# Kernel tuning notes

Measured on AMD Instinct MI355X. Metric: run time of the kernel, lower is better.

Reference implementation:

```python
import jax, jax.numpy as jnp
import numpy as np

D_MODEL = 1024
N_HEADS = 16
HEAD_DIM = D_MODEL // N_HEADS
BATCH = 4
SEQ = 2048


def setup_inputs() -> dict:
    key = jax.random.key(0)
    k_x, k_wqkv, k_bqkv, k_wo, k_bo = jax.random.split(key, 5)
    x = jax.random.normal(k_x, (BATCH, SEQ, D_MODEL), dtype=jnp.float32)
    # causal mask: True = masked (upper triangle, excluding diagonal)
    mask = jnp.triu(jnp.ones((SEQ, SEQ), dtype=bool), k=1)
    lim = 1.0 / np.sqrt(D_MODEL)
    w_qkv = jax.random.uniform(k_wqkv, (D_MODEL, 3 * D_MODEL), jnp.float32, -lim, lim)
    b_qkv = jax.random.uniform(k_bqkv, (3 * D_MODEL,), jnp.float32, -lim, lim)
    w_out = jax.random.uniform(k_wo, (D_MODEL, D_MODEL), jnp.float32, -lim, lim)
    b_out = jax.random.uniform(k_bo, (D_MODEL,), jnp.float32, -lim, lim)
    return {"x": x, "mask": mask, "w_qkv": w_qkv, "b_qkv": b_qkv,
            "w_out": w_out, "b_out": b_out}


def reference(x, mask, w_qkv, b_qkv, w_out, b_out):
    b, s, _ = x.shape
    scale = HEAD_DIM ** -0.5
    qkv = x @ w_qkv + b_qkv                          # [b, s, 3*d]
    qkv = qkv.reshape(b, s, 3, N_HEADS, HEAD_DIM)
    qkv = jnp.transpose(qkv, (2, 0, 3, 1, 4))        # [3, b, h, s, hd]
    q, k, v = qkv[0], qkv[1], qkv[2]
    attn = jnp.einsum('bhqd,bhkd->bhqk', q, k) * scale
    attn = jnp.where(mask, -jnp.inf, attn)
    attn = jax.nn.softmax(attn, axis=-1)
    out = jnp.einsum('bhqk,bhkd->bhqd', attn, v)     # [b, h, s, hd]
    out = jnp.transpose(out, (0, 2, 1, 3)).reshape(b, s, D_MODEL)
    return out @ w_out + b_out
```

## Files before the change

kernel.cpp:

```cpp
#include <hip/hip_runtime.h>
#include <stdint.h>

typedef unsigned short u16;
typedef __attribute__((ext_vector_type(8))) short short8;
typedef __attribute__((ext_vector_type(4))) float f32x4;
typedef __attribute__((ext_vector_type(16))) float f32x16;

#define DEV static __device__ __forceinline__

#define QSCALE 0.18033688011112042f

DEV float fast_exp2(float x) { return __builtin_amdgcn_exp2f(x); }

DEV float bf2f(u16 u) { union { uint32_t i; float f; } x; x.i = ((uint32_t)u) << 16; return x.f; }
DEV u16 f2bf(float f) {
  union { float f; uint32_t i; } x; x.f = f;
  uint32_t r = x.i + 0x7FFFu + ((x.i >> 16) & 1u);
  return (u16)(r >> 16);
}
DEV uint32_t pk_bf16(float lo, float hi) {
  uint32_t r;
  asm("v_cvt_pk_bf16_f32 %0, %1, %2" : "=v"(r) : "v"(lo), "v"(hi));
  return r;
}

DEV void async_copy16(void* lds_dst, const void* gsrc) {
  typedef __attribute__((address_space(1))) void* gp_t;
  typedef __attribute__((address_space(3))) void* lp_t;
  __builtin_amdgcn_global_load_lds((gp_t)(uintptr_t)gsrc,
                                   (lp_t)(uint32_t)(uintptr_t)lds_dst, 16, 0, 0);
}

DEV void gemm_bt_core(const u16* __restrict__ A, const u16* __restrict__ Bt, int K,
                      int m0, int n0, uint8_t* As, uint8_t* Bs,
                      f32x4 (&acc)[4][4], int wave, int lane, int wm, int wn) {
#pragma unroll
  for (int mt = 0; mt < 4; ++mt)
#pragma unroll
    for (int nt = 0; nt < 4; ++nt)
      acc[mt][nt] = (f32x4){0.f, 0.f, 0.f, 0.f};

  for (int k0 = 0; k0 < K; k0 += 64) {
    __syncthreads();
#pragma unroll
    for (int i = 0; i < 4; ++i) {
      int cb = wave * 256 + i * 64;
      int c  = cb + lane;
      int r  = c >> 3;
      int ks = (c & 7) ^ (r & 7);
      async_copy16(As + cb * 16 + lane * 16, A  + (size_t)(m0 + r) * K + k0 + ks * 8);
      async_copy16(Bs + cb * 16 + lane * 16, Bt + (size_t)(n0 + r) * K + k0 + ks * 8);
    }
    __syncthreads();

    short8 af[2][4], bf_[2][4];
#pragma unroll
    for (int kk = 0; kk < 2; ++kk)
#pragma unroll
      for (int t = 0; t < 4; ++t) {
        int ra = wm + t * 16 + (lane & 15);
        af[kk][t]  = *(const short8*)(As + ra * 128 + (((kk * 4 + (lane >> 4)) ^ (ra & 7)) << 4));
        int rb = wn + t * 16 + (lane & 15);
        bf_[kk][t] = *(const short8*)(Bs + rb * 128 + (((kk * 4 + (lane >> 4)) ^ (rb & 7)) << 4));
      }
#pragma unroll
    for (int kk = 0; kk < 2; ++kk)
#pragma unroll
      for (int mt = 0; mt < 4; ++mt)
#pragma unroll
        for (int nt = 0; nt < 4; ++nt)
          acc[mt][nt] = __builtin_amdgcn_mfma_f32_16x16x32_bf16(af[kk][mt], bf_[kk][nt],
                                                                acc[mt][nt], 0, 0, 0);
  }
}

__global__ __launch_bounds__(256, 2) void k_gemm_qkv(
    const u16* __restrict__ X, const u16* __restrict__ WT, const float* __restrict__ bias,
    u16* __restrict__ Q, u16* __restrict__ Kv, u16* __restrict__ Vt) {
  __shared__ __attribute__((aligned(16))) uint8_t As[16384];
  __shared__ __attribute__((aligned(16))) uint8_t Bs[16384];
  const int lane = threadIdx.x & 63, wave = threadIdx.x >> 6;
  const int wm = (wave >> 1) * 64, wn = (wave & 1) * 64;
  const int m0 = blockIdx.x * 128, n0 = blockIdx.y * 128;
  f32x4 acc[4][4];
  gemm_bt_core(X, WT, 1024, m0, n0, As, Bs, acc, wave, lane, wm, wn);
#pragma unroll
  for (int nt = 0; nt < 4; ++nt) {
    int n = n0 + wn + nt * 16 + (lane & 15);
    float bv = bias[n];
    int which = n >> 10, h = (n >> 6) & 15, hd = n & 63;
    if (which == 2) {
#pragma unroll
      for (int mt = 0; mt < 4; ++mt) {
        int m = m0 + wm + mt * 16 + (lane >> 4) * 4;
        int b = m >> 11, s = m & 2047;
        u16 tmp[4];
#pragma unroll
        for (int rg = 0; rg < 4; ++rg) tmp[rg] = f2bf(acc[mt][nt][rg] + bv);
        *(uint64_t*)(Vt + ((size_t)(b * 16 + h) * 64 + hd) * 2048 + s) = *(const uint64_t*)tmp;
      }
    } else {
      u16* base = (which == 0) ? Q : Kv;
      const float mul = (which == 0) ? QSCALE : 1.0f;
#pragma unroll
      for (int mt = 0; mt < 4; ++mt)
#pragma unroll
        for (int rg = 0; rg < 4; ++rg) {
          int m = m0 + wm + mt * 16 + (lane >> 4) * 4 + rg;
          int b = m >> 11, s = m & 2047;
          base[((size_t)(b * 16 + h) * 2048 + s) * 64 + hd] = f2bf((acc[mt][nt][rg] + bv) * mul);
        }
    }
  }
}

__global__ __launch_bounds__(256, 2) void k_gemm_out(
    const u16* __restrict__ A, const u16* __restrict__ WT, const float* __restrict__ bias,
    float* __restrict__ Out) {
  __shared__ __attribute__((aligned(16))) uint8_t As[16384];
  __shared__ __attribute__((aligned(16))) uint8_t Bs[16384];
  const int lane = threadIdx.x & 63, wave = threadIdx.x >> 6;
  const int wm = (wave >> 1) * 64, wn = (wave & 1) * 64;
  const int m0 = blockIdx.x * 128, n0 = blockIdx.y * 128;
  f32x4 acc[4][4];
  gemm_bt_core(A, WT, 1024, m0, n0, As, Bs, acc, wave, lane, wm, wn);
#pragma unroll
  for (int nt = 0; nt < 4; ++nt) {
    int n = n0 + wn + nt * 16 + (lane & 15);
    float bv = bias[n];
#pragma unroll
    for (int mt = 0; mt < 4; ++mt)
#pragma unroll
      for (int rg = 0; rg < 4; ++rg) {
        int m = m0 + wm + mt * 16 + (lane >> 4) * 4 + rg;
        Out[(size_t)m * 1024 + n] = acc[mt][nt][rg] + bv;
      }
  }
}

__global__ __launch_bounds__(256) void k_cvt_x(const float* __restrict__ src,
                                               u16* __restrict__ dst, int n8) {
  int i = blockIdx.x * 256 + threadIdx.x;
  if (i >= n8) return;
  float4 a = *(const float4*)(src + (size_t)i * 8);
  float4 b = *(const float4*)(src + (size_t)i * 8 + 4);
  u16 tmp[8] = {f2bf(a.x), f2bf(a.y), f2bf(a.z), f2bf(a.w),
                f2bf(b.x), f2bf(b.y), f2bf(b.z), f2bf(b.w)};
  *(short8*)(dst + (size_t)i * 8) = *(const short8*)tmp;
}

__global__ __launch_bounds__(256) void k_transpose_f32(
    const float* __restrict__ src, u16* __restrict__ dst, int R, int C) {
  __shared__ u16 tile[64][72];
  const int tr = blockIdx.x * 64, tc = blockIdx.y * 64;
  for (int c = threadIdx.x; c < 1024; c += 256) {
    int r = c >> 4, c4 = (c & 15) * 4;
    float4 v = *(const float4*)(src + (size_t)(tr + r) * C + tc + c4);
    tile[r][c4 + 0] = f2bf(v.x); tile[r][c4 + 1] = f2bf(v.y);
    tile[r][c4 + 2] = f2bf(v.z); tile[r][c4 + 3] = f2bf(v.w);
  }
  __syncthreads();
  for (int c = threadIdx.x; c < 512; c += 256) {
    int oc = c >> 3, r8 = (c & 7) * 8;
    u16 tmp[8];
#pragma unroll
    for (int i = 0; i < 8; ++i) tmp[i] = tile[r8 + i][oc];
    *(short8*)(dst + (size_t)(tc + oc) * R + tr + r8) = *(const short8*)tmp;
  }
}

DEV void stage_tile(const u16* __restrict__ Kg, const u16* __restrict__ Vg,
                    uint8_t* kb, uint8_t* vb, int t, int tid) {
#pragma unroll
  for (int i = 0; i < 2; ++i) {
    int c = i * 256 + tid;
    int r = c >> 3;
    int ks = (c & 7) ^ (r & 7);
    async_copy16(kb + c * 16, Kg + (size_t)(t * 64 + r) * 64 + ks * 8);
    async_copy16(vb + c * 16, Vg + (size_t)r * 2048 + t * 64 + ks * 8);
  }
}

__global__ __launch_bounds__(256, 2) void k_attn(
    const u16* __restrict__ Q, const u16* __restrict__ K,
    const u16* __restrict__ Vt, u16* __restrict__ O) {
  __shared__ __attribute__((aligned(16))) uint8_t kbuf[2][8192];
  __shared__ __attribute__((aligned(16))) uint8_t vbuf[2][8192];
  const int tid = threadIdx.x;
  const int lane = tid & 63;
  const int wave = tid >> 6;
  const int q32 = lane & 31, hv = lane >> 5;
  const float NEG_INF = -__builtin_inff();

  int L = blockIdx.x;
  int bh = (L & 7) * 8 + ((L >> 3) >> 3);
  int pair = (L >> 3) & 7;
  const int b = bh >> 4, h = bh & 15;
  const size_t hb = (size_t)bh * (2048 * 64);
  const u16* Qg = Q + hb;
  const u16* Kg = K + hb;
  const u16* Vg = Vt + hb;

#pragma unroll 1
  for (int which = 0; which < 2; ++which) {
    const int s = which ? (15 - pair) : pair;
    const int nt = 2 * (s + 1);
    const int qbase = s * 128 + wave * 32;
    const int qg = qbase + q32;
    const int my_nt = ((qbase + 31) >> 6) + 1;

    short8 qf[4];
#pragma unroll
    for (int dblk = 0; dblk < 4; ++dblk)
      qf[dblk] = *(const short8*)(Qg + (size_t)qg * 64 + dblk * 16 + hv * 8);

    f32x16 oacc[2] = {};
    float mrun = NEG_INF, lrun = 0.f;

    stage_tile(Kg, Vg, kbuf[0], vbuf[0], 0, tid);
    __syncthreads();

#pragma unroll 1
    for (int t = 0; t < nt; ++t) {
      const int cur = t & 1;
      if (t + 1 < nt) stage_tile(Kg, Vg, kbuf[cur ^ 1], vbuf[cur ^ 1], t + 1, tid);

      if (t < my_nt) {
        const uint8_t* kb = kbuf[cur];
        const uint8_t* vb = vbuf[cur];

        f32x16 sa0 = {}, sa1 = {};
        __builtin_amdgcn_s_setprio(1);
#pragma unroll
        for (int dblk = 0; dblk < 4; ++dblk) {
          short8 kf0 = *(const short8*)(kb + q32 * 128 + (((dblk * 2 + hv) ^ (q32 & 7)) << 4));
          short8 kf1 = *(const short8*)(kb + (32 + q32) * 128 + (((dblk * 2 + hv) ^ (q32 & 7)) << 4));
          sa0 = __builtin_amdgcn_mfma_f32_32x32x16_bf16(kf0, qf[dblk], sa0, 0, 0, 0);
          sa1 = __builtin_amdgcn_mfma_f32_32x32x16_bf16(kf1, qf[dblk], sa1, 0, 0, 0);
        }
        __builtin_amdgcn_s_setprio(0);

        float sv[32];
#pragma unroll
        for (int r = 0; r < 16; ++r) { sv[r] = sa0[r]; sv[16 + r] = sa1[r]; }
        if (t * 64 + 63 > qbase) {
#pragma unroll
          for (int r = 0; r < 16; ++r) {
            int kl = (r & 3) + 8 * (r >> 2) + 4 * hv;
            if (t * 64 + kl > qg)      sv[r]      = NEG_INF;
            if (t * 64 + 32 + kl > qg) sv[16 + r] = NEG_INF;
          }
        }

        float mloc = fmaxf(sv[0], sv[1]);
#pragma unroll
        for (int r = 2; r < 32; ++r) mloc = fmaxf(mloc, sv[r]);
        float mtile = fmaxf(mloc, __shfl_xor(mloc, 32, 64));
        if (!__all(mtile <= mrun + 8.f)) {
          float mnew = fmaxf(mrun, mtile);
          float corr = fast_exp2(mrun - mnew);
          mrun = mnew;
          lrun *= corr;
#pragma unroll
          for (int r = 0; r < 16; ++r) { oacc[0][r] *= corr; oacc[1][r] *= corr; }
        }
        float ls = 0.f;
#pragma unroll
        for (int r = 0; r < 32; ++r) { sv[r] = fast_exp2(sv[r] - mrun); ls += sv[r]; }
        ls += __shfl_xor(ls, 32, 64);
        lrun += ls;

        __builtin_amdgcn_s_setprio(1);
#pragma unroll
        for (int ksub = 0; ksub < 2; ++ksub) {
#pragma unroll
          for (int kb2 = 0; kb2 < 2; ++kb2) {
            const int rb = ksub * 16 + kb2 * 8;
            uint32_t pA = pk_bf16(sv[rb + 0], sv[rb + 1]);
            uint32_t pB = pk_bf16(sv[rb + 2], sv[rb + 3]);
            uint32_t pC = pk_bf16(sv[rb + 4], sv[rb + 5]);
            uint32_t pD = pk_bf16(sv[rb + 6], sv[rb + 7]);
            uint32_t X = hv ? pA : pC;
            uint32_t Y = hv ? pB : pD;
            uint32_t sX = (uint32_t)__shfl_xor((int)X, 32, 64);
            uint32_t sY = (uint32_t)__shfl_xor((int)Y, 32, 64);
            union { uint32_t u[4]; short8 s8; } pu;
            pu.u[0] = hv ? sX : pA;
            pu.u[1] = hv ? sY : pB;
            pu.u[2] = hv ? pC : sX;
            pu.u[3] = hv ? pD : sY;
            const int kblk = ksub * 2 + kb2;
            short8 vf0 = *(const short8*)(vb + q32 * 128 + (((kblk * 2 + hv) ^ (q32 & 7)) << 4));
            short8 vf1 = *(const short8*)(vb + (32 + q32) * 128 + (((kblk * 2 + hv) ^ (q32 & 7)) << 4));
            oacc[0] = __builtin_amdgcn_mfma_f32_32x32x16_bf16(vf0, pu.s8, oacc[0], 0, 0, 0);
            oacc[1] = __builtin_amdgcn_mfma_f32_32x32x16_bf16(vf1, pu.s8, oacc[1], 0, 0, 0);
          }
        }
        __builtin_amdgcn_s_setprio(0);
      }

      __syncthreads();
    }

    float rl = 1.0f / lrun;
    u16* orow = O + ((size_t)(b * 2048 + qg)) * 1024 + h * 64;
#pragma unroll
    for (int dt = 0; dt < 2; ++dt)
#pragma unroll
      for (int g = 0; g < 4; ++g) {
        int dbase = dt * 32 + 8 * g + 4 * hv;
        u16 tmp[4];
#pragma unroll
        for (int j = 0; j < 4; ++j) tmp[j] = f2bf(oacc[dt][4 * g + j] * rl);
        *(uint64_t*)(orow + dbase) = *(const uint64_t*)tmp;
      }
  }
}

extern "C" void kernel_launch(void* const* d_in, const int* in_sizes, int n_in,
                              void* d_out, int out_size, void* d_ws, size_t ws_size,
                              hipStream_t stream) {
  const float* x     = (const float*)d_in[0];
  const float* w_qkv = (const float*)d_in[2];
  const float* b_qkv = (const float*)d_in[3];
  const float* w_out = (const float*)d_in[4];
  const float* b_out = (const float*)d_in[5];
  float* out = (float*)d_out;
  uint8_t* ws = (uint8_t*)d_ws;

  u16* wqkvT = (u16*)(ws);
  u16* woutT = (u16*)(ws +  6291456);
  u16* Xb    = (u16*)(ws +  8388608);
  u16* Qb    = (u16*)(ws + 25165824);
  u16* Kb    = (u16*)(ws + 41943040);
  u16* Vtb   = (u16*)(ws + 58720256);
  u16* AO    = Xb;

  k_cvt_x<<<dim3(4096), 256, 0, stream>>>(x, Xb, 1048576);
  k_transpose_f32<<<dim3(16, 48), 256, 0, stream>>>(w_qkv, wqkvT, 1024, 3072);
  k_transpose_f32<<<dim3(16, 16), 256, 0, stream>>>(w_out, woutT, 1024, 1024);
  k_gemm_qkv<<<dim3(64, 24), 256, 0, stream>>>(Xb, wqkvT, b_qkv, Qb, Kb, Vtb);
  k_attn<<<dim3(512), 256, 0, stream>>>(Qb, Kb, Vtb, AO);
  k_gemm_out<<<dim3(64, 8), 256, 0, stream>>>(AO, woutT, b_out, out);
}
```

Baseline: 154.3 us.

## Use 256x128 GEMM tiles with triple-buffered async LDS pipeline

```diff
diff --git a/kernel.cpp b/kernel.cpp
--- a/kernel.cpp
+++ b/kernel.cpp
@@ -31,109 +31,142 @@
                                    (lp_t)(uint32_t)(uintptr_t)lds_dst, 16, 0, 0);
 }
 
-DEV void gemm_bt_core(const u16* __restrict__ A, const u16* __restrict__ Bt, int K,
-                      int m0, int n0, uint8_t* As, uint8_t* Bs,
-                      f32x4 (&acc)[4][4], int wave, int lane, int wm, int wn) {
-#pragma unroll
-  for (int mt = 0; mt < 4; ++mt)
-#pragma unroll
-    for (int nt = 0; nt < 4; ++nt)
-      acc[mt][nt] = (f32x4){0.f, 0.f, 0.f, 0.f};
-
-  for (int k0 = 0; k0 < K; k0 += 64) {
-    __syncthreads();
-#pragma unroll
-    for (int i = 0; i < 4; ++i) {
-      int cb = wave * 256 + i * 64;
-      int c  = cb + lane;
-      int r  = c >> 3;
-      int ks = (c & 7) ^ (r & 7);
-      async_copy16(As + cb * 16 + lane * 16, A  + (size_t)(m0 + r) * K + k0 + ks * 8);
-      async_copy16(Bs + cb * 16 + lane * 16, Bt + (size_t)(n0 + r) * K + k0 + ks * 8);
+#define SLOT_BYTES 49152
+
+DEV void stage_slot(const u16* __restrict__ A, const u16* __restrict__ Bt,
+                    int m0, int n0, int k0, uint8_t* As, uint8_t* Bs, int tid) {
+#pragma unroll
+  for (int i = 0; i < 4; ++i) {
+    int c = i * 512 + tid;
+    int r = c >> 3;
+    int ks = (c & 7) ^ (r & 7);
+    async_copy16(As + c * 16, A + (size_t)(m0 + r) * 1024 + k0 + ks * 8);
+  }
+#pragma unroll
+  for (int i = 0; i < 2; ++i) {
+    int c = i * 512 + tid;
+    int r = c >> 3;
+    int ks = (c & 7) ^ (r & 7);
+    async_copy16(Bs + c * 16, Bt + (size_t)(n0 + r) * 1024 + k0 + ks * 8);
+  }
+}
+
+DEV void gemm256_core(const u16* __restrict__ A, const u16* __restrict__ Bt,
+                      int m0, int n0, uint8_t* lds,
+                      f32x4 (&acc)[4][4], int wave, int lane, int tid) {
+  const int wm = (wave >> 1) * 64, wn = (wave & 1) * 64;
+#pragma unroll
+  for (int mf = 0; mf < 4; ++mf)
+#pragma unroll
+    for (int nf = 0; nf < 4; ++nf)
+      acc[mf][nf] = (f32x4){0.f, 0.f, 0.f, 0.f};
+
+  stage_slot(A, Bt, m0, n0, 0,  lds,              lds + 32768,              tid);
+  stage_slot(A, Bt, m0, n0, 64, lds + SLOT_BYTES, lds + SLOT_BYTES + 32768, tid);
+
+  int cur = 0;
+#pragma unroll 1
+  for (int kt = 0; kt < 16; ++kt) {
+    if (kt + 2 < 16) {
+      int nxt = (cur >= 1) ? cur - 1 : 2;
+      stage_slot(A, Bt, m0, n0, (kt + 2) * 64,
+                 lds + nxt * SLOT_BYTES, lds + nxt * SLOT_BYTES + 32768, tid);
     }
-    __syncthreads();
-
-    short8 af[2][4], bf_[2][4];
-#pragma unroll
-    for (int kk = 0; kk < 2; ++kk)
-#pragma unroll
-      for (int t = 0; t < 4; ++t) {
-        int ra = wm + t * 16 + (lane & 15);
-        af[kk][t]  = *(const short8*)(As + ra * 128 + (((kk * 4 + (lane >> 4)) ^ (ra & 7)) << 4));
-        int rb = wn + t * 16 + (lane & 15);
-        bf_[kk][t] = *(const short8*)(Bs + rb * 128 + (((kk * 4 + (lane >> 4)) ^ (rb & 7)) << 4));
-      }
-#pragma unroll
-    for (int kk = 0; kk < 2; ++kk)
-#pragma unroll
-      for (int mt = 0; mt < 4; ++mt)
-#pragma unroll
-        for (int nt = 0; nt < 4; ++nt)
-          acc[mt][nt] = __builtin_amdgcn_mfma_f32_16x16x32_bf16(af[kk][mt], bf_[kk][nt],
-                                                                acc[mt][nt], 0, 0, 0);
-  }
-}
-
-__global__ __launch_bounds__(256, 2) void k_gemm_qkv(
+    if (kt < 14)       asm volatile("s_waitcnt vmcnt(12)" ::: "memory");
+    else if (kt == 14) asm volatile("s_waitcnt vmcnt(6)"  ::: "memory");
+    else               asm volatile("s_waitcnt vmcnt(0)"  ::: "memory");
+    asm volatile("s_barrier" ::: "memory");
+
+    const uint8_t* Ab = lds + cur * SLOT_BYTES;
+    const uint8_t* Bb = Ab + 32768;
+#pragma unroll
+    for (int kk = 0; kk < 2; ++kk) {
+      short8 af[4], bfr[4];
+#pragma unroll
+      for (int f = 0; f < 4; ++f) {
+        int ra = wm + f * 16 + (lane & 15);
+        af[f]  = *(const short8*)(Ab + ra * 128 + (((kk * 4 + (lane >> 4)) ^ (ra & 7)) << 4));
+      }
+#pragma unroll
+      for (int f = 0; f < 4; ++f) {
+        int rb = wn + f * 16 + (lane & 15);
+        bfr[f] = *(const short8*)(Bb + rb * 128 + (((kk * 4 + (lane >> 4)) ^ (rb & 7)) << 4));
+      }
+      asm volatile("s_barrier" ::: "memory");
+      asm volatile("s_waitcnt lgkmcnt(0)" ::: "memory");
+      __builtin_amdgcn_sched_barrier(0);
+      __builtin_amdgcn_s_setprio(1);
+#pragma unroll
+      for (int mf = 0; mf < 4; ++mf)
+#pragma unroll
+        for (int nf = 0; nf < 4; ++nf)
+          acc[mf][nf] = __builtin_amdgcn_mfma_f32_16x16x32_bf16(af[mf], bfr[nf],
+                                                                acc[mf][nf], 0, 0, 0);
+      __builtin_amdgcn_s_setprio(0);
+      asm volatile("s_barrier" ::: "memory");
+    }
+    cur = (cur == 2) ? 0 : cur + 1;
+  }
+}
+
+__global__ __launch_bounds__(512, 2) void k_gemm_qkv(
     const u16* __restrict__ X, const u16* __restrict__ WT, const float* __restrict__ bias,
     u16* __restrict__ Q, u16* __restrict__ Kv, u16* __restrict__ Vt) {
-  __shared__ __attribute__((aligned(16))) uint8_t As[16384];
-  __shared__ __attribute__((aligned(16))) uint8_t Bs[16384];
-  const int lane = threadIdx.x & 63, wave = threadIdx.x >> 6;
+  __shared__ __attribute__((aligned(16))) uint8_t lds[3 * SLOT_BYTES];
+  const int tid = threadIdx.x, lane = tid & 63, wave = tid >> 6;
   const int wm = (wave >> 1) * 64, wn = (wave & 1) * 64;
-  const int m0 = blockIdx.x * 128, n0 = blockIdx.y * 128;
+  const int m0 = blockIdx.x * 256, n0 = blockIdx.y * 128;
   f32x4 acc[4][4];
-  gemm_bt_core(X, WT, 1024, m0, n0, As, Bs, acc, wave, lane, wm, wn);
-#pragma unroll
-  for (int nt = 0; nt < 4; ++nt) {
-    int n = n0 + wn + nt * 16 + (lane & 15);
+  gemm256_core(X, WT, m0, n0, lds, acc, wave, lane, tid);
+#pragma unroll
+  for (int nf = 0; nf < 4; ++nf) {
+    int n = n0 + wn + nf * 16 + (lane & 15);
     float bv = bias[n];
     int which = n >> 10, h = (n >> 6) & 15, hd = n & 63;
     if (which == 2) {
 #pragma unroll
-      for (int mt = 0; mt < 4; ++mt) {
-        int m = m0 + wm + mt * 16 + (lane >> 4) * 4;
+      for (int mf = 0; mf < 4; ++mf) {
+        int m = m0 + wm + mf * 16 + (lane >> 4) * 4;
         int b = m >> 11, s = m & 2047;
         u16 tmp[4];
 #pragma unroll
-        for (int rg = 0; rg < 4; ++rg) tmp[rg] = f2bf(acc[mt][nt][rg] + bv);
+        for (int rg = 0; rg < 4; ++rg) tmp[rg] = f2bf(acc[mf][nf][rg] + bv);
         *(uint64_t*)(Vt + ((size_t)(b * 16 + h) * 64 + hd) * 2048 + s) = *(const uint64_t*)tmp;
       }
     } else {
       u16* base = (which == 0) ? Q : Kv;
       const float mul = (which == 0) ? QSCALE : 1.0f;
 #pragma unroll
-      for (int mt = 0; mt < 4; ++mt)
+      for (int mf = 0; mf < 4; ++mf)
 #pragma unroll
         for (int rg = 0; rg < 4; ++rg) {
-          int m = m0 + wm + mt * 16 + (lane >> 4) * 4 + rg;
+          int m = m0 + wm + mf * 16 + (lane >> 4) * 4 + rg;
           int b = m >> 11, s = m & 2047;
-          base[((size_t)(b * 16 + h) * 2048 + s) * 64 + hd] = f2bf((acc[mt][nt][rg] + bv) * mul);
+          base[((size_t)(b * 16 + h) * 2048 + s) * 64 + hd] = f2bf((acc[mf][nf][rg] + bv) * mul);
         }
     }
   }
 }
 
-__global__ __launch_bounds__(256, 2) void k_gemm_out(
+__global__ __launch_bounds__(512, 2) void k_gemm_out(
     const u16* __restrict__ A, const u16* __restrict__ WT, const float* __restrict__ bias,
     float* __restrict__ Out) {
-  __shared__ __attribute__((aligned(16))) uint8_t As[16384];
-  __shared__ __attribute__((aligned(16))) uint8_t Bs[16384];
-  const int lane = threadIdx.x & 63, wave = threadIdx.x >> 6;
+  __shared__ __attribute__((aligned(16))) uint8_t lds[3 * SLOT_BYTES];
+  const int tid = threadIdx.x, lane = tid & 63, wave = tid >> 6;
   const int wm = (wave >> 1) * 64, wn = (wave & 1) * 64;
-  const int m0 = blockIdx.x * 128, n0 = blockIdx.y * 128;
+  const int m0 = blockIdx.x * 256, n0 = blockIdx.y * 128;
   f32x4 acc[4][4];
-  gemm_bt_core(A, WT, 1024, m0, n0, As, Bs, acc, wave, lane, wm, wn);
-#pragma unroll
-  for (int nt = 0; nt < 4; ++nt) {
-    int n = n0 + wn + nt * 16 + (lane & 15);
+  gemm256_core(A, WT, m0, n0, lds, acc, wave, lane, tid);
+#pragma unroll
+  for (int nf = 0; nf < 4; ++nf) {
+    int n = n0 + wn + nf * 16 + (lane & 15);
     float bv = bias[n];
 #pragma unroll
-    for (int mt = 0; mt < 4; ++mt)
+    for (int mf = 0; mf < 4; ++mf)
 #pragma unroll
       for (int rg = 0; rg < 4; ++rg) {
-        int m = m0 + wm + mt * 16 + (lane >> 4) * 4 + rg;
-        Out[(size_t)m * 1024 + n] = acc[mt][nt][rg] + bv;
+        int m = m0 + wm + mf * 16 + (lane >> 4) * 4 + rg;
+        Out[(size_t)m * 1024 + n] = acc[mf][nf][rg] + bv;
       }
   }
 }
@@ -311,7 +344,7 @@
         int dbase = dt * 32 + 8 * g + 4 * hv;
         u16 tmp[4];
 #pragma unroll
-        for (int j = 0; j < 4; ++j) tmp[j] = f2bf(oacc[dt][4 * g + j] * rl);
+        for (int j2 = 0; j2 < 4; ++j2) tmp[j2] = f2bf(oacc[dt][4 * g + j2] * rl);
         *(uint64_t*)(orow + dbase) = *(const uint64_t*)tmp;
       }
   }
@@ -339,7 +372,7 @@
   k_cvt_x<<<dim3(4096), 256, 0, stream>>>(x, Xb, 1048576);
   k_transpose_f32<<<dim3(16, 48), 256, 0, stream>>>(w_qkv, wqkvT, 1024, 3072);
   k_transpose_f32<<<dim3(16, 16), 256, 0, stream>>>(w_out, woutT, 1024, 1024);
-  k_gemm_qkv<<<dim3(64, 24), 256, 0, stream>>>(Xb, wqkvT, b_qkv, Qb, Kb, Vtb);
+  k_gemm_qkv<<<dim3(32, 24), 512, 0, stream>>>(Xb, wqkvT, b_qkv, Qb, Kb, Vtb);
   k_attn<<<dim3(512), 256, 0, stream>>>(Qb, Kb, Vtb, AO);
-  k_gemm_out<<<dim3(64, 8), 256, 0, stream>>>(AO, woutT, b_out, out);
-}
+  k_gemm_out<<<dim3(32, 8), 512, 0, stream>>>(AO, woutT, b_out, out);
+}
```

Result: slower. 168.3 us (+9.0%).
